# Kernel optimization log

Hardware: AMD Instinct MI355X
Metric: run time of the kernel (lower is better)

The kernel has to match this reference:

```python
import jax, jax.numpy as jnp
import numpy as np
from jax import lax

B, S, D, V, MAXLEN = 32, 2048, 1024, 32000, 2048
EPS = jnp.finfo(jnp.float32).eps  # torch RMSNorm default eps=None -> finfo eps


def setup_inputs() -> dict:
    key = jax.random.key(0)
    ks = jax.random.split(key, 10)
    w = lambda k, shape: (jax.random.normal(k, shape, jnp.float32) * 0.02)
    return {
        "x": jax.random.randint(ks[0], (B, S), 0, V),
        "emb": w(ks[1], (V, D)),
        "pos": w(ks[2], (MAXLEN, D)),
        "conv_w": w(ks[3], (3, D, D)),            # HIO layout (k, in, out)
        "conv_b": jnp.zeros((D,), jnp.float32),
        "wg1": w(ks[4], (D, D)), "bg1": jnp.zeros((D,), jnp.float32),
        "wmv": w(ks[5], (2 * D, D)), "bmv": jnp.zeros((D,), jnp.float32),
        "wmg": w(ks[6], (2 * D, D)), "bmg": jnp.zeros((D,), jnp.float32),
        "wrg": w(ks[7], (2 * D, D)), "brg": jnp.zeros((D,), jnp.float32),
        "rms_w": jnp.ones((D,), jnp.float32),
        "wp": w(ks[8], (2 * D, V)), "bp": jnp.zeros((V,), jnp.float32),
    }


def _rmsnorm(v, rms_w):
    ms = jnp.mean(v * v, axis=-1, keepdims=True)
    return v * lax.rsqrt(ms + EPS) * rms_w


def reference(x, emb, pos, conv_w, conv_b, wg1, bg1, wmv, bmv, wmg, bmg,
              wrg, brg, rms_w, wp, bp):
    seq_len = x.shape[1]
    h = emb[x] + pos[:seq_len]                     # [B, S, D]
    # Conv1d(D, D, k=3, padding=1) over the sequence axis
    h = lax.conv_general_dilated(h, conv_w, window_strides=(1,),
                                 padding=((1, 1),),
                                 dimension_numbers=("NHC", "HIO", "NHC")) + conv_b
    nodes = h * jax.nn.sigmoid(h @ wg1 + bg1)      # gated nodes [B, S, D]

    curr = nodes[:, :-1, :]                        # nodes_past [B, S-1, D]
    while curr.shape[1] > 1:                       # log2(S) static levels
        if curr.shape[1] % 2 != 0:
            curr = jnp.concatenate([curr, curr[:, -1:, :]], axis=1)
        left = curr[:, 0::2, :]
        right = curr[:, 1::2, :]
        combined = jnp.concatenate([left, right], axis=-1)   # [B, n/2, 2D]
        val = combined @ wmv + bmv
        gate = jax.nn.sigmoid(combined @ wmg + bmg)
        merged = _rmsnorm(val * gate, rms_w)
        res_gate = jax.nn.sigmoid(combined @ wrg + brg)
        residual = (left + right) * 0.5
        curr = res_gate * merged + (1.0 - res_gate) * residual

    root = curr[:, 0, :]                           # [B, D]
    last = nodes[:, -2, :]                         # last of nodes_past
    context = jnp.concatenate([root, last], axis=-1)  # [B, 2D]
    return context @ wp + bp                       # logits [B, V]
```

## Files before the change

### kernel.cpp

```cpp
#include <hip/hip_runtime.h>
#include <stdint.h>

typedef __bf16 bf16_t;
typedef __attribute__((ext_vector_type(8))) __bf16 bf16x8;
typedef __attribute__((ext_vector_type(4))) __bf16 bf16x4;
typedef __attribute__((ext_vector_type(4))) float f32x4;

#define NB 32
#define NS 2048
#define ND 1024
#define NV 32000
#define SP 2050

__device__ __forceinline__ float sigmoid_(float x) { return 1.0f / (1.0f + __expf(-x)); }

__device__ __forceinline__ void gload_lds16(const void* g, void* lds) {
  __builtin_amdgcn_global_load_lds((const __attribute__((address_space(1))) void*)g,
                                   (__attribute__((address_space(3))) void*)lds, 16, 0, 0);
}


__global__ void zero_pad_k(bf16_t* h0p) {
  int i = blockIdx.x;
  int b = i >> 1;
  size_t row = (size_t)b * SP + ((i & 1) ? (SP - 1) : 0);
  bf16x4 z = {};
  *(bf16x4*)(h0p + row * ND + threadIdx.x * 4) = z;
}

__global__ void embed_k(const int* __restrict__ x, const float* __restrict__ emb,
                        const float* __restrict__ pos, bf16_t* __restrict__ h0p) {
  int bs = blockIdx.x;
  int b = bs >> 11, s = bs & (NS - 1);
  int idx = x[bs];
  const float* e = emb + (size_t)idx * ND;
  const float* p = pos + (size_t)s * ND;
  bf16_t* o = h0p + ((size_t)b * SP + s + 1) * ND;
  int d = threadIdx.x * 4;
  f32x4 ev = *(const f32x4*)(e + d);
  f32x4 pv = *(const f32x4*)(p + d);
  bf16x4 ov;
  ov[0] = (bf16_t)(ev[0] + pv[0]);
  ov[1] = (bf16_t)(ev[1] + pv[1]);
  ov[2] = (bf16_t)(ev[2] + pv[2]);
  ov[3] = (bf16_t)(ev[3] + pv[3]);
  *(bf16x4*)(o + d) = ov;
}

__global__ void conv_transpose_k(const float* __restrict__ in, bf16_t* __restrict__ out,
                                 int R, int C) {
  __shared__ float tile[32][33];
  int tc = blockIdx.x * 32, tr = blockIdx.y * 32;
  int tx = threadIdx.x;
  for (int i = threadIdx.y; i < 32; i += 8)
    tile[i][tx] = in[(size_t)(tr + i) * C + tc + tx];
  __syncthreads();
  for (int i = threadIdx.y; i < 32; i += 8)
    out[(size_t)(tc + i) * R + tr + tx] = (bf16_t)tile[tx][i];
}

__global__ void dup_row_k(bf16_t* nodes) {
  int b = blockIdx.x;
  const bf16_t* src = nodes + ((size_t)b * NS + NS - 2) * ND;
  bf16_t* dst = nodes + ((size_t)b * NS + NS - 1) * ND;
  int d = threadIdx.x * 4;
  *(bf16x4*)(dst + d) = *(const bf16x4*)(src + d);
}

__global__ void concat3_k(const float* __restrict__ a, const float* __restrict__ b,
                          const float* __restrict__ c, float* __restrict__ o) {
  int i = blockIdx.x * 256 + threadIdx.x;
  o[i] = i < 1024 ? a[i] : (i < 2048 ? b[i - 1024] : c[i - 2048]);
}

template <int EPI>
__global__ __launch_bounds__(512, 2) void gemm256(
    const bf16_t* __restrict__ A, const bf16_t* __restrict__ Bt,
    const float* __restrict__ bias, const void* aux, void* Cout,
    int M, int N, int K, int lda, int batchShift, int batchPad,
    int GX, int gpx, int nxg, int ych) {
  const int tid = threadIdx.x;
  const int lane = tid & 63;
  const int wave = tid >> 6;
  int n0, m0;
  if (nxg == 0) {
    n0 = (blockIdx.x % GX) * 256;
    m0 = (blockIdx.x / GX) * 256;
  } else {
    const int id = blockIdx.x;
    const int xcd = id & 7;
    const int jb = id >> 3;
    const int xg = xcd % nxg;
    const int ysub = xcd / nxg;
    n0 = (xg * gpx + (jb % gpx)) * 256;
    m0 = (ysub * ych + (jb / gpx)) * 256;
  }
  const int waveM = wave >> 2, waveN = wave & 3;

  __shared__ __align__(16) bf16_t sA[2][256 * 64];
  __shared__ __align__(16) bf16_t sB[2][256 * 64];

  const int srow = tid >> 3;
  const int sj = tid & 7;
  const bf16_t* pA[4];
  const bf16_t* pB[4];
#pragma unroll
  for (int idx = 0; idx < 4; ++idx) {
    int lr = idx * 64 + srow;
    int sc = sj ^ (lr & 7);
    int gm = m0 + lr;
    if (gm > M - 1) gm = M - 1;
    size_t grow = (size_t)gm + (size_t)(((unsigned)gm) >> batchShift) * batchPad;
    pA[idx] = A + grow * (size_t)lda + sc * 8;
    int gn = n0 + lr;
    if (gn > N - 1) gn = N - 1;
    pB[idx] = Bt + (size_t)gn * K + sc * 8;
  }
  const int ldsrow = wave * 8;

  auto stageA4 = [&](int buf) {
#pragma unroll
    for (int idx = 0; idx < 4; ++idx) {
      gload_lds16(pA[idx], &sA[buf][(size_t)(idx * 64 + ldsrow) * 64]);
      pA[idx] += 64;
    }
  };
  auto stageB2 = [&](int buf, int half) {
#pragma unroll
    for (int r = 0; r < 2; ++r) {
      int idx = half * 2 + r;
      gload_lds16(pB[idx], &sB[buf][(size_t)(idx * 64 + ldsrow) * 64]);
      pB[idx] += 64;
    }
  };

  const int rlane = lane & 15;
  const int klane = lane >> 4;
  int offA[8][2], offB[4][2];
#pragma unroll
  for (int i = 0; i < 8; ++i) {
    int ra = waveM * 128 + i * 16 + rlane;
#pragma unroll
    for (int ks = 0; ks < 2; ++ks)
      offA[i][ks] = ra * 128 + (((ks * 4 + klane) ^ (ra & 7)) << 4);
  }
#pragma unroll
  for (int j = 0; j < 4; ++j) {
    int rb = waveN * 64 + j * 16 + rlane;
#pragma unroll
    for (int ks = 0; ks < 2; ++ks)
      offB[j][ks] = rb * 128 + (((ks * 4 + klane) ^ (rb & 7)) << 4);
  }

  f32x4 acc[8][4] = {};

  const int nt = K >> 6;
  stageA4(0);
  stageB2(0, 0); stageB2(0, 1);
  stageB2(1, 0); stageB2(1, 1);
  asm volatile("s_waitcnt vmcnt(4)" ::: "memory");
  __builtin_amdgcn_s_barrier();

  for (int tt = 0; tt < nt; tt += 2) {
#pragma unroll
    for (int u = 0; u < 2; ++u) {
      const int t = tt + u;
      bf16x8 bfr[4][2];
#pragma unroll
      for (int p = 0; p < 4; ++p) {
        if (p == 0) {
#pragma unroll
          for (int j = 0; j < 4; ++j)
#pragma unroll
            for (int ks = 0; ks < 2; ++ks)
              bfr[j][ks] = *(const bf16x8*)((const char*)&sB[u][0] + offB[j][ks]);
        }
        bf16x8 af[2][2];
#pragma unroll
        for (int ii = 0; ii < 2; ++ii)
#pragma unroll
          for (int ks = 0; ks < 2; ++ks)
            af[ii][ks] = *(const bf16x8*)((const char*)&sA[u][0] + offA[p * 2 + ii][ks]);
        if (p == 0) {
          if (t + 1 < nt) stageA4(u ^ 1);
        } else if (p == 1) {
          if (t + 2 < nt) stageB2(u, 0);
        } else if (p == 2) {
          if (t + 2 < nt) stageB2(u, 1);
        }
        __builtin_amdgcn_s_barrier();
        __builtin_amdgcn_s_setprio(1);
#pragma unroll
        for (int ks = 0; ks < 2; ++ks)
#pragma unroll
          for (int ii = 0; ii < 2; ++ii)
#pragma unroll
            for (int j = 0; j < 4; ++j)
              acc[p * 2 + ii][j] = __builtin_amdgcn_mfma_f32_16x16x32_bf16(
                  af[ii][ks], bfr[j][ks], acc[p * 2 + ii][j], 0, 0, 0);
        __builtin_amdgcn_s_setprio(0);
        if (p < 3) {
          __builtin_amdgcn_s_barrier();
        } else {
          if (t + 2 < nt)
            asm volatile("s_waitcnt vmcnt(4)" ::: "memory");
          else
            asm volatile("s_waitcnt vmcnt(0)" ::: "memory");
          __builtin_amdgcn_s_barrier();
        }
      }
    }
  }

  const int colBase = n0 + waveN * 64 + rlane;
#pragma unroll
  for (int i = 0; i < 8; ++i) {
    const int rowBase = m0 + waveM * 128 + i * 16 + klane * 4;
#pragma unroll
    for (int j = 0; j < 4; ++j) {
      const int col = colBase + j * 16;
      const float bv = bias[col];
#pragma unroll
      for (int r = 0; r < 4; ++r) {
        const int row = rowBase + r;
        if (row >= M) continue;
        float v = acc[i][j][r] + bv;
        size_t o = (size_t)row * N + col;
        if constexpr (EPI == 0) {
          ((bf16_t*)Cout)[o] = (bf16_t)v;
        } else if constexpr (EPI == 1) {
          float hh = (float)((const bf16_t*)aux)[o];
          ((bf16_t*)Cout)[o] = (bf16_t)(hh * sigmoid_(v));
        } else {
          ((bf16_t*)Cout)[o] = (bf16_t)(col < 1024 ? v : sigmoid_(v));
        }
      }
    }
  }
}

template <bool ATOMIC>
__global__ __launch_bounds__(256, 2) void gemm128s(
    const bf16_t* __restrict__ A, const bf16_t* __restrict__ Bt,
    const float* __restrict__ bias, float* __restrict__ Cout,
    int M, int kLen, int nxy) {
  const int tid = threadIdx.x;
  const int lane = tid & 63;
  const int wave = tid >> 6;
  const int id = blockIdx.x;
  const int sk = id / nxy;
  const int rb2 = id % nxy;
  const int n0 = (rb2 % 24) * 128;
  const int m0 = (rb2 / 24) * 128;
  const int kOff = sk * kLen;

  const int waveM = wave >> 1, waveN = wave & 1;

  __shared__ __align__(16) bf16_t sA[2][128 * 64];
  __shared__ __align__(16) bf16_t sB[2][128 * 64];

  f32x4 acc[4][4] = {};

  const int srow = wave * 8 + (lane >> 3);
  const int sj = lane & 7;

  auto stage = [&](int buf, int kk0) {
#pragma unroll
    for (int j = 0; j < 4; ++j) {
      int rowT = j * 32 + srow;
      int k8 = sj ^ (rowT & 7);
      int gm = m0 + rowT;
      if (gm > M - 1) gm = M - 1;
      gload_lds16(A + (size_t)gm * 2048 + (kk0 + k8 * 8), &sA[buf][(j * 256 + wave * 64) * 8]);
      int gn = n0 + rowT;
      gload_lds16(Bt + (size_t)gn * 2048 + (kk0 + k8 * 8), &sB[buf][(j * 256 + wave * 64) * 8]);
    }
  };

  stage(0, kOff);
  __syncthreads();

  const int nt = kLen >> 6;
  int cur = 0;
  const int ar = waveM * 64 + (lane & 15);
  const int br = waveN * 64 + (lane & 15);
  const int kb0 = lane >> 4;

  for (int t = 0; t < nt; ++t) {
    if (t + 1 < nt) stage(cur ^ 1, kOff + (t + 1) * 64);

    const bf16_t* sa = sA[cur];
    const bf16_t* sb = sB[cur];
    bf16x8 af[2][4], bfr[2][4];
#pragma unroll
    for (int ks = 0; ks < 2; ++ks) {
      int kb = kb0 + ks * 4;
#pragma unroll
      for (int i = 0; i < 4; ++i) {
        int ra = ar + i * 16;
        af[ks][i] = *(const bf16x8*)&sa[ra * 64 + ((kb ^ (ra & 7)) * 8)];
        int rbq = br + i * 16;
        bfr[ks][i] = *(const bf16x8*)&sb[rbq * 64 + ((kb ^ (rbq & 7)) * 8)];
      }
    }
#pragma unroll
    for (int ks = 0; ks < 2; ++ks)
#pragma unroll
      for (int i = 0; i < 4; ++i)
#pragma unroll
        for (int j = 0; j < 4; ++j)
          acc[i][j] = __builtin_amdgcn_mfma_f32_16x16x32_bf16(af[ks][i], bfr[ks][j], acc[i][j], 0, 0, 0);
    __syncthreads();
    cur ^= 1;
  }

  const int colBase = n0 + waveN * 64 + (lane & 15);
#pragma unroll
  for (int i = 0; i < 4; ++i) {
    const int rowBase = m0 + waveM * 64 + i * 16 + (lane >> 4) * 4;
#pragma unroll
    for (int jj = 0; jj < 4; ++jj) {
      const int col = colBase + jj * 16;
      const float bv = (!ATOMIC || kOff == 0) ? bias[col] : 0.0f;
#pragma unroll
      for (int r = 0; r < 4; ++r) {
        const int row = rowBase + r;
        if (row >= M) continue;
        float v = acc[i][jj][r] + bv;
        size_t o = (size_t)row * 3072 + col;
        if constexpr (ATOMIC)
          atomicAdd(&Cout[o], v);
        else
          Cout[o] = v;
      }
    }
  }
}

__global__ __launch_bounds__(256) void tree_combine_k(
    const bf16_t* __restrict__ fb, const bf16_t* __restrict__ cur,
    const float* __restrict__ rms_w, bf16_t* __restrict__ outb) {
  const int m = blockIdx.x;
  const int t = threadIdx.x;
  const int d = t * 4;
  const bf16_t* row = fb + (size_t)m * 3072;
  bf16x4 vb = *(const bf16x4*)(row + d);
  bf16x4 gb = *(const bf16x4*)(row + 1024 + d);
  bf16x4 rb = *(const bf16x4*)(row + 2048 + d);
  f32x4 vg;
#pragma unroll
  for (int k = 0; k < 4; ++k) vg[k] = (float)vb[k] * (float)gb[k];
  float ss = vg[0] * vg[0] + vg[1] * vg[1] + vg[2] * vg[2] + vg[3] * vg[3];
#pragma unroll
  for (int o = 32; o > 0; o >>= 1) ss += __shfl_xor(ss, o);
  __shared__ float red[4];
  if ((t & 63) == 0) red[t >> 6] = ss;
  __syncthreads();
  float ms = (red[0] + red[1] + red[2] + red[3]) * (1.0f / ND);
  float scale = rsqrtf(ms + 1.1920929e-07f);
  f32x4 w = *(const f32x4*)(rms_w + d);
  const bf16_t* c0 = cur + (size_t)m * 2048;
  bf16x4 lv = *(const bf16x4*)(c0 + d);
  bf16x4 rv = *(const bf16x4*)(c0 + ND + d);
  bf16x4 o4;
#pragma unroll
  for (int k = 0; k < 4; ++k) {
    float merged = vg[k] * scale * w[k];
    float resid = 0.5f * ((float)lv[k] + (float)rv[k]);
    float g = (float)rb[k];
    o4[k] = (bf16_t)(g * merged + (1.0f - g) * resid);
  }
  *(bf16x4*)(outb + (size_t)m * ND + d) = o4;
}

__global__ __launch_bounds__(256) void tree_combine32_k(
    const float* __restrict__ fb, const bf16_t* __restrict__ cur,
    const float* __restrict__ rms_w, bf16_t* __restrict__ outb) {
  const int m = blockIdx.x;
  const int t = threadIdx.x;
  const int d = t * 4;
  const float* row = fb + (size_t)m * 3072;
  f32x4 v = *(const f32x4*)(row + d);
  f32x4 gl = *(const f32x4*)(row + 1024 + d);
  f32x4 rl = *(const f32x4*)(row + 2048 + d);
  f32x4 vg;
#pragma unroll
  for (int k = 0; k < 4; ++k) vg[k] = v[k] * sigmoid_(gl[k]);
  float ss = vg[0] * vg[0] + vg[1] * vg[1] + vg[2] * vg[2] + vg[3] * vg[3];
#pragma unroll
  for (int o = 32; o > 0; o >>= 1) ss += __shfl_xor(ss, o);
  __shared__ float red[4];
  if ((t & 63) == 0) red[t >> 6] = ss;
  __syncthreads();
  float ms = (red[0] + red[1] + red[2] + red[3]) * (1.0f / ND);
  float scale = rsqrtf(ms + 1.1920929e-07f);
  f32x4 w = *(const f32x4*)(rms_w + d);
  const bf16_t* c0 = cur + (size_t)m * 2048;
  bf16x4 lv = *(const bf16x4*)(c0 + d);
  bf16x4 rv = *(const bf16x4*)(c0 + ND + d);
  bf16x4 o4;
#pragma unroll
  for (int k = 0; k < 4; ++k) {
    float merged = vg[k] * scale * w[k];
    float resid = 0.5f * ((float)lv[k] + (float)rv[k]);
    float g = sigmoid_(rl[k]);
    o4[k] = (bf16_t)(g * merged + (1.0f - g) * resid);
  }
  *(bf16x4*)(outb + (size_t)m * ND + d) = o4;
}

__global__ void build_ctx_k(const bf16_t* __restrict__ root, const bf16_t* __restrict__ nodes,
                            float* __restrict__ ctx) {
  int b = blockIdx.x, t = threadIdx.x;
  const bf16_t* r = root + (size_t)b * ND;
  const bf16_t* l = nodes + ((size_t)b * NS + NS - 2) * ND;
  int d = t * 4;
#pragma unroll
  for (int k = 0; k < 4; ++k) {
    ctx[(size_t)b * 2048 + d + k] = (float)r[d + k];
    ctx[(size_t)b * 2048 + ND + d + k] = (float)l[d + k];
  }
}

__global__ __launch_bounds__(256) void final_proj_k(
    const float* __restrict__ ctx, const float* __restrict__ wp,
    const float* __restrict__ bp, float* __restrict__ out) {
  const int v = blockIdx.x * 256 + threadIdx.x;
  float acc[NB];
#pragma unroll
  for (int b = 0; b < NB; ++b) acc[b] = 0.f;
  __shared__ float sctx[NB][128];
  for (int k0 = 0; k0 < 2048; k0 += 128) {
    __syncthreads();
    for (int i = threadIdx.x; i < NB * 128; i += 256) {
      int bb = i >> 7, kk = i & 127;
      sctx[bb][kk] = ctx[(size_t)bb * 2048 + k0 + kk];
    }
    __syncthreads();
    for (int kk = 0; kk < 128; ++kk) {
      float wv = wp[(size_t)(k0 + kk) * NV + v];
#pragma unroll
      for (int b = 0; b < NB; ++b) acc[b] += sctx[b][kk] * wv;
    }
  }
#pragma unroll
  for (int b = 0; b < NB; ++b) out[(size_t)b * NV + v] = acc[b] + bp[v];
}

extern "C" void kernel_launch(void* const* d_in, const int* in_sizes, int n_in,
                              void* d_out, int out_size, void* d_ws, size_t ws_size,
                              hipStream_t stream) {
  const int* x = (const int*)d_in[0];
  const float* emb = (const float*)d_in[1];
  const float* pos = (const float*)d_in[2];
  const float* conv_w = (const float*)d_in[3];
  const float* conv_b = (const float*)d_in[4];
  const float* wg1 = (const float*)d_in[5];
  const float* bg1 = (const float*)d_in[6];
  const float* wmv = (const float*)d_in[7];
  const float* bmv = (const float*)d_in[8];
  const float* wmg = (const float*)d_in[9];
  const float* bmg = (const float*)d_in[10];
  const float* wrg = (const float*)d_in[11];
  const float* brg = (const float*)d_in[12];
  const float* rms_w = (const float*)d_in[13];
  const float* wp = (const float*)d_in[14];
  const float* bp = (const float*)d_in[15];
  float* out = (float*)d_out;

  char* ws = (char*)d_ws;
  size_t off = 0;
  auto alloc = [&](size_t bytes) -> void* {
    void* p = ws + off;
    off += (bytes + 255) & ~(size_t)255;
    return p;
  };
  bf16_t* h0p = (bf16_t*)alloc((size_t)NB * SP * ND * 2);
  bf16_t* h = (bf16_t*)alloc((size_t)NB * NS * ND * 2);
  bf16_t* nodes = (bf16_t*)alloc((size_t)NB * NS * ND * 2);
  bf16_t* tb0 = (bf16_t*)alloc((size_t)NB * 1024 * ND * 2);
  bf16_t* tb1 = (bf16_t*)alloc((size_t)NB * 1024 * ND * 2);
  bf16_t* convT = (bf16_t*)alloc((size_t)ND * 3072 * 2);
  bf16_t* wg1T = (bf16_t*)alloc((size_t)ND * 1024 * 2);
  bf16_t* wAllT = (bf16_t*)alloc((size_t)3072 * 2048 * 2);
  float* bAll = (float*)alloc((size_t)3072 * 4);
  float* ctx = (float*)alloc((size_t)NB * 2048 * 4);
  if (off > ws_size) return;
  bf16_t* fbuf = (bf16_t*)ws;
  float* fbuf32 = (float*)ws;

  dim3 t256(256), tb32(32, 8);

  conv_transpose_k<<<dim3(ND / 32, 3072 / 32), tb32, 0, stream>>>(conv_w, convT, 3072, ND);
  conv_transpose_k<<<dim3(ND / 32, ND / 32), tb32, 0, stream>>>(wg1, wg1T, ND, ND);
  conv_transpose_k<<<dim3(ND / 32, 2048 / 32), tb32, 0, stream>>>(wmv, wAllT, 2048, ND);
  conv_transpose_k<<<dim3(ND / 32, 2048 / 32), tb32, 0, stream>>>(wmg, wAllT + (size_t)1024 * 2048, 2048, ND);
  conv_transpose_k<<<dim3(ND / 32, 2048 / 32), tb32, 0, stream>>>(wrg, wAllT + (size_t)2048 * 2048, 2048, ND);
  concat3_k<<<12, t256, 0, stream>>>(bmv, bmg, brg, bAll);

  zero_pad_k<<<64, t256, 0, stream>>>(h0p);
  embed_k<<<NB * NS, t256, 0, stream>>>(x, emb, pos, h0p);

  gemm256<0><<<1024, 512, 0, stream>>>(h0p, convT, conv_b, nullptr, h,
                                       NB * NS, ND, 3072, ND, 11, 2, 4, 1, 4, 128);
  gemm256<1><<<1024, 512, 0, stream>>>(h, wg1T, bg1, h, nodes,
                                       NB * NS, ND, ND, ND, 0, 0, 4, 1, 4, 128);
  dup_row_k<<<NB, t256, 0, stream>>>(nodes);

  const bf16_t* cur = nodes;
  bf16_t* bufs[2] = {tb0, tb1};
  int pp = 0;
  for (int L = NS; L > 1; L >>= 1) {
    int M = NB * (L / 2);
    if (M >= 16384) {
      int GY = M / 256;
      gemm256<3><<<12 * GY, 512, 0, stream>>>(cur, wAllT, bAll, nullptr, fbuf,
                                              M, 3072, 2048, 2048, 0, 0, 12, 3, 4, GY / 2);
      tree_combine_k<<<M, t256, 0, stream>>>(fbuf, cur, rms_w, bufs[pp]);
    } else {
      int GY = (M + 127) / 128;
      int nxy = 24 * GY;
      int SK = 1;
      while (nxy * SK < 768 && SK < 16) SK <<= 1;
      if (SK > 1) {
        hipMemsetAsync(fbuf32, 0, (size_t)M * 3072 * 4, stream);
        gemm128s<true><<<nxy * SK, t256, 0, stream>>>(cur, wAllT, bAll, fbuf32,
                                                      M, 2048 / SK, nxy);
      } else {
        gemm128s<false><<<nxy, t256, 0, stream>>>(cur, wAllT, bAll, fbuf32, M, 2048, nxy);
      }
      tree_combine32_k<<<M, t256, 0, stream>>>(fbuf32, cur, rms_w, bufs[pp]);
    }
    cur = bufs[pp];
    pp ^= 1;
  }

  build_ctx_k<<<NB, t256, 0, stream>>>(cur, nodes, ctx);
  final_proj_k<<<NV / 256, t256, 0, stream>>>(ctx, wp, bp, out);
}
```

Before: 2.689 ms.

## Restructure GEMM main loop into two phases and move final projection to MFMA

The 256-wide GEMM inner loop is reorganized from four barrier-separated quarter phases into two halves per k-tile. It uses a single barrier and issues all A and B staging loads at once, which reduces synchronization overhead. The final vocabulary projection moves from a scalar FP32 kernel to a bf16 MFMA kernel over a transposed copy of wp. That kernel splits K four ways, accumulates with atomics, and adds a bias-initialization kernel. This adds a per-call transpose of the 2048x32000 weight and lowers the projection's precision to bf16.

```diff
diff --git a/kernel.cpp b/kernel.cpp
--- a/kernel.cpp
+++ b/kernel.cpp
@@ -125,10 +125,9 @@
       pA[idx] += 64;
     }
   };
-  auto stageB2 = [&](int buf, int half) {
-#pragma unroll
-    for (int r = 0; r < 2; ++r) {
-      int idx = half * 2 + r;
+  auto stageB4 = [&](int buf) {
+#pragma unroll
+    for (int idx = 0; idx < 4; ++idx) {
       gload_lds16(pB[idx], &sB[buf][(size_t)(idx * 64 + ldsrow) * 64]);
       pB[idx] += 64;
     }
@@ -156,8 +155,8 @@
 
   const int nt = K >> 6;
   stageA4(0);
-  stageB2(0, 0); stageB2(0, 1);
-  stageB2(1, 0); stageB2(1, 1);
+  stageB4(0);
+  stageB4(1);
   asm volatile("s_waitcnt vmcnt(4)" ::: "memory");
   __builtin_amdgcn_s_barrier();
 
@@ -167,48 +166,52 @@
       const int t = tt + u;
       bf16x8 bfr[4][2];
 #pragma unroll
-      for (int p = 0; p < 4; ++p) {
-        if (p == 0) {
+      for (int j = 0; j < 4; ++j)
+#pragma unroll
+        for (int ks = 0; ks < 2; ++ks)
+          bfr[j][ks] = *(const bf16x8*)((const char*)&sB[u][0] + offB[j][ks]);
+      asm volatile("" ::: "memory");
+      bf16x8 a0[4][2];
+#pragma unroll
+      for (int i = 0; i < 4; ++i)
+#pragma unroll
+        for (int ks = 0; ks < 2; ++ks)
+          a0[i][ks] = *(const bf16x8*)((const char*)&sA[u][0] + offA[i][ks]);
+      asm volatile("s_waitcnt lgkmcnt(8)" ::: "memory");
+      __builtin_amdgcn_s_barrier();
+      if (t + 1 < nt) stageA4(u ^ 1);
+      if (t + 2 < nt) stageB4(u);
+      __builtin_amdgcn_s_setprio(1);
+#pragma unroll
+      for (int ks = 0; ks < 2; ++ks)
+#pragma unroll
+        for (int i = 0; i < 4; ++i)
 #pragma unroll
           for (int j = 0; j < 4; ++j)
-#pragma unroll
-            for (int ks = 0; ks < 2; ++ks)
-              bfr[j][ks] = *(const bf16x8*)((const char*)&sB[u][0] + offB[j][ks]);
-        }
-        bf16x8 af[2][2];
-#pragma unroll
-        for (int ii = 0; ii < 2; ++ii)
-#pragma unroll
-          for (int ks = 0; ks < 2; ++ks)
-            af[ii][ks] = *(const bf16x8*)((const char*)&sA[u][0] + offA[p * 2 + ii][ks]);
-        if (p == 0) {
-          if (t + 1 < nt) stageA4(u ^ 1);
-        } else if (p == 1) {
-          if (t + 2 < nt) stageB2(u, 0);
-        } else if (p == 2) {
-          if (t + 2 < nt) stageB2(u, 1);
-        }
-        __builtin_amdgcn_s_barrier();
-        __builtin_amdgcn_s_setprio(1);
+            acc[i][j] = __builtin_amdgcn_mfma_f32_16x16x32_bf16(
+                a0[i][ks], bfr[j][ks], acc[i][j], 0, 0, 0);
+      __builtin_amdgcn_s_setprio(0);
+      bf16x8 a1[4][2];
+#pragma unroll
+      for (int i = 0; i < 4; ++i)
 #pragma unroll
         for (int ks = 0; ks < 2; ++ks)
-#pragma unroll
-          for (int ii = 0; ii < 2; ++ii)
-#pragma unroll
-            for (int j = 0; j < 4; ++j)
-              acc[p * 2 + ii][j] = __builtin_amdgcn_mfma_f32_16x16x32_bf16(
-                  af[ii][ks], bfr[j][ks], acc[p * 2 + ii][j], 0, 0, 0);
-        __builtin_amdgcn_s_setprio(0);
-        if (p < 3) {
-          __builtin_amdgcn_s_barrier();
-        } else {
-          if (t + 2 < nt)
-            asm volatile("s_waitcnt vmcnt(4)" ::: "memory");
-          else
-            asm volatile("s_waitcnt vmcnt(0)" ::: "memory");
-          __builtin_amdgcn_s_barrier();
-        }
-      }
+          a1[i][ks] = *(const bf16x8*)((const char*)&sA[u][0] + offA[4 + i][ks]);
+      __builtin_amdgcn_s_setprio(1);
+#pragma unroll
+      for (int ks = 0; ks < 2; ++ks)
+#pragma unroll
+        for (int i = 0; i < 4; ++i)
+#pragma unroll
+          for (int j = 0; j < 4; ++j)
+            acc[4 + i][j] = __builtin_amdgcn_mfma_f32_16x16x32_bf16(
+                a1[i][ks], bfr[j][ks], acc[4 + i][j], 0, 0, 0);
+      __builtin_amdgcn_s_setprio(0);
+      if (t + 2 < nt)
+        asm volatile("s_waitcnt vmcnt(4)" ::: "memory");
+      else
+        asm volatile("s_waitcnt vmcnt(0)" ::: "memory");
+      __builtin_amdgcn_s_barrier();
     }
   }
 
@@ -410,41 +413,56 @@
 }
 
 __global__ void build_ctx_k(const bf16_t* __restrict__ root, const bf16_t* __restrict__ nodes,
-                            float* __restrict__ ctx) {
+                            bf16_t* __restrict__ ctxb) {
   int b = blockIdx.x, t = threadIdx.x;
   const bf16_t* r = root + (size_t)b * ND;
   const bf16_t* l = nodes + ((size_t)b * NS + NS - 2) * ND;
   int d = t * 4;
-#pragma unroll
-  for (int k = 0; k < 4; ++k) {
-    ctx[(size_t)b * 2048 + d + k] = (float)r[d + k];
-    ctx[(size_t)b * 2048 + ND + d + k] = (float)l[d + k];
-  }
-}
-
-__global__ __launch_bounds__(256) void final_proj_k(
-    const float* __restrict__ ctx, const float* __restrict__ wp,
-    const float* __restrict__ bp, float* __restrict__ out) {
-  const int v = blockIdx.x * 256 + threadIdx.x;
-  float acc[NB];
-#pragma unroll
-  for (int b = 0; b < NB; ++b) acc[b] = 0.f;
-  __shared__ float sctx[NB][128];
-  for (int k0 = 0; k0 < 2048; k0 += 128) {
-    __syncthreads();
-    for (int i = threadIdx.x; i < NB * 128; i += 256) {
-      int bb = i >> 7, kk = i & 127;
-      sctx[bb][kk] = ctx[(size_t)bb * 2048 + k0 + kk];
-    }
-    __syncthreads();
-    for (int kk = 0; kk < 128; ++kk) {
-      float wv = wp[(size_t)(k0 + kk) * NV + v];
-#pragma unroll
-      for (int b = 0; b < NB; ++b) acc[b] += sctx[b][kk] * wv;
-    }
-  }
-#pragma unroll
-  for (int b = 0; b < NB; ++b) out[(size_t)b * NV + v] = acc[b] + bp[v];
+  *(bf16x4*)(ctxb + (size_t)b * 2048 + d) = *(const bf16x4*)(r + d);
+  *(bf16x4*)(ctxb + (size_t)b * 2048 + ND + d) = *(const bf16x4*)(l + d);
+}
+
+__global__ void init_out_k(const float* __restrict__ bp, float* __restrict__ out) {
+  int i = blockIdx.x * 256 + threadIdx.x;
+  int b = i / NV;
+  out[i] = bp[i - b * NV];
+}
+
+__global__ __launch_bounds__(256) void proj_gemm_k(
+    const bf16_t* __restrict__ ctxb, const bf16_t* __restrict__ wpT,
+    float* __restrict__ out) {
+  const int lane = threadIdx.x & 63;
+  const int wave = threadIdx.x >> 6;
+  const int n0 = blockIdx.x * 256 + wave * 64;
+  const int kbase = blockIdx.y * 512;
+  const int rl = lane & 15, kl = lane >> 4;
+  f32x4 acc[2][4] = {};
+#pragma unroll 4
+  for (int kt = 0; kt < 16; ++kt) {
+    const int k0 = kbase + kt * 32 + kl * 8;
+    bf16x8 af[2], bfr[4];
+#pragma unroll
+    for (int i = 0; i < 2; ++i)
+      af[i] = *(const bf16x8*)&ctxb[(size_t)(i * 16 + rl) * 2048 + k0];
+#pragma unroll
+    for (int j = 0; j < 4; ++j)
+      bfr[j] = *(const bf16x8*)&wpT[(size_t)(n0 + j * 16 + rl) * 2048 + k0];
+#pragma unroll
+    for (int i = 0; i < 2; ++i)
+#pragma unroll
+      for (int j = 0; j < 4; ++j)
+        acc[i][j] = __builtin_amdgcn_mfma_f32_16x16x32_bf16(af[i], bfr[j], acc[i][j], 0, 0, 0);
+  }
+#pragma unroll
+  for (int i = 0; i < 2; ++i)
+#pragma unroll
+    for (int j = 0; j < 4; ++j)
+#pragma unroll
+      for (int r = 0; r < 4; ++r) {
+        int b = i * 16 + kl * 4 + r;
+        int v = n0 + j * 16 + rl;
+        atomicAdd(&out[(size_t)b * NV + v], acc[i][j][r]);
+      }
 }
 
 extern "C" void kernel_launch(void* const* d_in, const int* in_sizes, int n_in,
@@ -484,10 +502,11 @@
   bf16_t* wg1T = (bf16_t*)alloc((size_t)ND * 1024 * 2);
   bf16_t* wAllT = (bf16_t*)alloc((size_t)3072 * 2048 * 2);
   float* bAll = (float*)alloc((size_t)3072 * 4);
-  float* ctx = (float*)alloc((size_t)NB * 2048 * 4);
+  bf16_t* ctxb = (bf16_t*)alloc((size_t)NB * 2048 * 2);
   if (off > ws_size) return;
   bf16_t* fbuf = (bf16_t*)ws;
   float* fbuf32 = (float*)ws;
+  bf16_t* wpT = (bf16_t*)ws;
 
   dim3 t256(256), tb32(32, 8);
 
@@ -535,6 +554,8 @@
     pp ^= 1;
   }
 
-  build_ctx_k<<<NB, t256, 0, stream>>>(cur, nodes, ctx);
-  final_proj_k<<<NV / 256, t256, 0, stream>>>(ctx, wp, bp, out);
-}
+  build_ctx_k<<<NB, t256, 0, stream>>>(cur, nodes, ctxb);
+  conv_transpose_k<<<dim3(NV / 32, 2048 / 32), tb32, 0, stream>>>(wp, wpT, 2048, NV);
+  init_out_k<<<NB * NV / 256, t256, 0, stream>>>(bp, out);
+  proj_gemm_k<<<dim3(NV / 256, 4), t256, 0, stream>>>(ctxb, wpT, out);
+}
```

Result: faster. 2.315 ms (-13.9%).
